# Kernel tuning notes

Hardware: AMD Instinct MI355X
Metric: run time of the kernel (lower is better)

## Reference

```python
import jax, jax.numpy as jnp
import numpy as np

DIM = 1024
HEADS = 16
HEAD_DIM = DIM // HEADS
SCALE = HEAD_DIM ** -0.5
EPS = 1e-5


def layernorm(x, g, b):
    mu = jnp.mean(x, axis=-1, keepdims=True)
    var = jnp.mean((x - mu) ** 2, axis=-1, keepdims=True)
    return (x - mu) * jax.lax.rsqrt(var + EPS) * g + b


def setup_inputs() -> dict:
    key = jax.random.key(0)
    ks = jax.random.split(key, 12)
    B, N = 2, 2048
    s = DIM ** -0.5
    return {
        "q": jax.random.normal(ks[0], (B, N, DIM), jnp.float32),
        "k": jax.random.normal(ks[1], (B, N, DIM), jnp.float32),
        "v": jax.random.normal(ks[2], (B, N, DIM), jnp.float32),
        "gq": jnp.ones((DIM,), jnp.float32), "bq_ln": jnp.zeros((DIM,), jnp.float32),
        "gk": jnp.ones((DIM,), jnp.float32), "bk_ln": jnp.zeros((DIM,), jnp.float32),
        "gv": jnp.ones((DIM,), jnp.float32), "bv_ln": jnp.zeros((DIM,), jnp.float32),
        "Wq": jax.random.normal(ks[3], (DIM, DIM), jnp.float32) * s,
        "bq": jnp.zeros((DIM,), jnp.float32),
        "Wk": jax.random.normal(ks[4], (DIM, DIM), jnp.float32) * s,
        "bk": jnp.zeros((DIM,), jnp.float32),
        "Wv": jax.random.normal(ks[5], (DIM, DIM), jnp.float32) * s,
        "bv": jnp.zeros((DIM,), jnp.float32),
        "Wp": jax.random.normal(ks[6], (DIM, DIM), jnp.float32) * s,
        "bp": jnp.zeros((DIM,), jnp.float32),
    }


def reference(q, k, v, gq, bq_ln, gk, bk_ln, gv, bv_ln, Wq, bq, Wk, bk, Wv, bv, Wp, bp):
    B, Nq, C = q.shape
    Nk, Nv = k.shape[1], v.shape[1]
    qn = layernorm(q, gq, bq_ln)
    kn = layernorm(k, gk, bk_ln)
    vn = layernorm(v, gv, bv_ln)
    # project and split heads -> [B, H, N, hd]
    qh = (qn @ Wq + bq).reshape(B, Nq, HEADS, HEAD_DIM).transpose(0, 2, 1, 3)
    kh = (kn @ Wk + bk).reshape(B, Nk, HEADS, HEAD_DIM).transpose(0, 2, 1, 3)
    vh = (vn @ Wv + bv).reshape(B, Nv, HEADS, HEAD_DIM).transpose(0, 2, 1, 3)
    attn = jnp.einsum("bhqd,bhkd->bhqk", qh, kh) * SCALE
    attn = jax.nn.softmax(attn, axis=-1)
    out = jnp.einsum("bhqk,bhkd->bhqd", attn, vh)
    out = out.transpose(0, 2, 1, 3).reshape(B, Nq, C)
    out = out @ Wp + bp
    return (out, kh, vh)
```

## Files before the change

kernel.cpp:

```cpp
#include <hip/hip_runtime.h>
#include <cstdint>

#define DIMC 1024
#define NSEQ 2048
#define BATCH 2
#define HEADS 16
#define HD 64
#define MROWS (BATCH * NSEQ)

typedef unsigned short u16;
typedef unsigned int u32;
typedef __attribute__((ext_vector_type(8))) short bf16x8;
typedef __attribute__((ext_vector_type(4))) float f32x4;

#if __has_builtin(__builtin_amdgcn_exp2f)
#define EXP2(x) __builtin_amdgcn_exp2f(x)
#else
#define EXP2(x) exp2f(x)
#endif

__device__ __forceinline__ u16 f2bf(float f) {
  union { float f; u32 u; } v; v.f = f;
  u32 u = v.u;
  return (u16)((u + 0x7fffu + ((u >> 16) & 1u)) >> 16);
}
__device__ __forceinline__ u32 pack_rne(float a, float b) {
  return (u32)f2bf(a) | ((u32)f2bf(b) << 16);
}
__device__ __forceinline__ u32 pack_trunc(float a, float b) {
  union { float f; u32 u; } x, y; x.f = a; y.f = b;
  return (x.u >> 16) | (y.u & 0xffff0000u);
}
__device__ __forceinline__ void gload_lds16(const void* g, void* l) {
  __builtin_amdgcn_global_load_lds((const __attribute__((address_space(1))) void*)g,
                                   (__attribute__((address_space(3))) void*)l, 16, 0, 0);
}

__global__ __launch_bounds__(256)
void prep(const float* __restrict__ q, const float* __restrict__ k,
          const float* __restrict__ v,
          const float* __restrict__ gq, const float* __restrict__ bq,
          const float* __restrict__ gk, const float* __restrict__ bk,
          const float* __restrict__ gv, const float* __restrict__ bv,
          const float* __restrict__ w0, const float* __restrict__ w1,
          const float* __restrict__ w2, const float* __restrict__ w3,
          u16* __restrict__ xn, u16* __restrict__ wtout) {
  __shared__ float rs[4], rs2[4];
  __shared__ float tile[32][33];
  int tid = threadIdx.x;
  if (blockIdx.x < 3 * MROWS) {
    int rowid = blockIdx.x;
    int tensor = rowid >> 12;
    int r = rowid & 4095;
    const float *src, *g, *b;
    if (tensor == 0)      { src = q; g = gq; b = bq; }
    else if (tensor == 1) { src = k; g = gk; b = bk; }
    else                  { src = v; g = gv; b = bv; }
    src += (size_t)r * DIMC;
    u16* dst = xn + (size_t)tensor * MROWS * DIMC + (size_t)r * DIMC;
    float4 x = ((const float4*)src)[tid];
    float s  = x.x + x.y + x.z + x.w;
    float s2 = x.x*x.x + x.y*x.y + x.z*x.z + x.w*x.w;
    #pragma unroll
    for (int m = 1; m < 64; m <<= 1) { s += __shfl_xor(s, m); s2 += __shfl_xor(s2, m); }
    int wave = tid >> 6, lane = tid & 63;
    if (lane == 0) { rs[wave] = s; rs2[wave] = s2; }
    __syncthreads();
    s  = rs[0] + rs[1] + rs[2] + rs[3];
    s2 = rs2[0] + rs2[1] + rs2[2] + rs2[3];
    float mu  = s * (1.0f / DIMC);
    float var = s2 * (1.0f / DIMC) - mu * mu;
    float inv = rsqrtf(var + 1e-5f);
    float4 gg = ((const float4*)g)[tid];
    float4 bb = ((const float4*)b)[tid];
    uint2 o;
    o.x = pack_rne((x.x - mu) * inv * gg.x + bb.x, (x.y - mu) * inv * gg.y + bb.y);
    o.y = pack_rne((x.z - mu) * inv * gg.z + bb.z, (x.w - mu) * inv * gg.w + bb.w);
    ((uint2*)dst)[tid] = o;
  } else {
    int blk = blockIdx.x - 3 * MROWS;
    int widx = blk >> 10, t = blk & 1023;
    int ti = t >> 5, tj = t & 31;
    const float* W = (widx == 0) ? w0 : (widx == 1) ? w1 : (widx == 2) ? w2 : w3;
    u16* O = wtout + (size_t)widx * DIMC * DIMC;
    int tx = tid & 31, ty = tid >> 5;
    #pragma unroll
    for (int rr = 0; rr < 32; rr += 8)
      tile[ty + rr][tx] = W[(size_t)(ti * 32 + ty + rr) * DIMC + tj * 32 + tx];
    __syncthreads();
    #pragma unroll
    for (int rr = 0; rr < 32; rr += 8)
      O[(size_t)(tj * 32 + ty + rr) * DIMC + ti * 32 + tx] = f2bf(tile[tx][ty + rr]);
  }
}

__global__ __launch_bounds__(256)
void qkv_gemm(const u16* __restrict__ xn, const u16* __restrict__ wt,
              const float* __restrict__ bq, const float* __restrict__ bk,
              const float* __restrict__ bv,
              float* __restrict__ out, u16* __restrict__ qh,
              u16* __restrict__ khb, u16* __restrict__ vtb) {
  __shared__ u16 smem[128 * 136];
  u16* As = smem;
  u16* Bs = smem + 4096;
  u16* Ls = smem;
  const int z = blockIdx.z;
  const u16* A  = xn + (size_t)z * MROWS * DIMC;
  const u16* Bt = wt + (size_t)z * DIMC * DIMC;
  const float* bias = (z == 0) ? bq : (z == 1) ? bk : bv;
  const int bm = blockIdx.x, bn = blockIdx.y;
  const int tid = threadIdx.x;
  const int wave = tid >> 6, lane = tid & 63;
  const int wm = (wave & 1) * 64, wn = (wave >> 1) * 64;
  const int row = lane & 15, quad = lane >> 4;
  const float QSCL = 0.18033688011112042f;
  f32x4 acc[4][4] = {};
  for (int k0 = 0; k0 < DIMC; k0 += 32) {
    #pragma unroll
    for (int c = 0; c < 2; ++c) {
      int e = c * 2048 + tid * 8;
      int rr = e >> 5, col = e & 31;
      gload_lds16(&A[(size_t)(bm * 128 + rr) * DIMC + k0 + col], &As[e]);
      gload_lds16(&Bt[(size_t)(bn * 128 + rr) * DIMC + k0 + col], &Bs[e]);
    }
    __syncthreads();
    bf16x8 a[4], b[4];
    #pragma unroll
    for (int i = 0; i < 4; ++i)
      a[i] = *(const bf16x8*)(&As[(wm + i * 16 + row) * 32 + quad * 8]);
    #pragma unroll
    for (int j = 0; j < 4; ++j)
      b[j] = *(const bf16x8*)(&Bs[(wn + j * 16 + row) * 32 + quad * 8]);
    #pragma unroll
    for (int i = 0; i < 4; ++i)
      #pragma unroll
      for (int j = 0; j < 4; ++j)
        acc[i][j] = __builtin_amdgcn_mfma_f32_16x16x32_bf16(a[i], b[j], acc[i][j], 0, 0, 0);
    __syncthreads();
  }
  #pragma unroll
  for (int i = 0; i < 4; ++i) {
    #pragma unroll
    for (int j = 0; j < 4; ++j) {
      float val[4];
      #pragma unroll
      for (int r = 0; r < 4; ++r) {
        int m = bm * 128 + wm + i * 16 + quad * 4 + r;
        int c = bn * 128 + wn + j * 16 + row;
        val[r] = acc[i][j][r] + bias[c];
        int b_ = m >> 11, n = m & 2047, h = c >> 6, d = c & 63;
        int bh = b_ * HEADS + h;
        size_t hidx = ((size_t)bh * NSEQ + n) * HD + d;
        if (z == 0) {
          qh[hidx] = f2bf(val[r] * QSCL);
        } else {
          out[(size_t)z * MROWS * DIMC + hidx] = val[r];
          if (z == 1) khb[hidx] = f2bf(val[r]);
        }
      }
      if (z == 2) {
        int ct = wn + j * 16 + row;
        int mt = wm + i * 16 + quad * 4;
        u32* L = (u32*)(&Ls[ct * 136 + mt]);
        L[0] = pack_rne(val[0], val[1]);
        L[1] = pack_rne(val[2], val[3]);
      }
    }
  }
  if (z == 2) {
    __syncthreads();
    int b_ = (bm * 128) >> 11;
    int nbase = (bm * 128) & 2047;
    #pragma unroll
    for (int it = 0; it < 8; ++it) {
      int idx = it * 256 + tid;
      int ct = idx >> 4, ch = idx & 15;
      uint4 y = *(const uint4*)(&Ls[ct * 136 + ch * 8]);
      int c = bn * 128 + ct;
      int h = c >> 6, d = c & 63;
      size_t o = ((size_t)(b_ * HEADS + h) * HD + d) * NSEQ + nbase + ch * 8;
      *(uint4*)(&vtb[o]) = y;
    }
  }
}

__global__ __launch_bounds__(256)
void out_gemm(const u16* __restrict__ A, const u16* __restrict__ Bt,
              const float* __restrict__ bias, float* __restrict__ outf) {
  __shared__ u16 As[64 * 32];
  __shared__ u16 Bs[128 * 32];
  const int bm = blockIdx.x, bn = blockIdx.y;
  const int tid = threadIdx.x;
  const int wave = tid >> 6, lane = tid & 63;
  const int wm = (wave & 1) * 32, wn = (wave >> 1) * 64;
  const int row = lane & 15, quad = lane >> 4;
  f32x4 acc[2][4] = {};
  for (int k0 = 0; k0 < DIMC; k0 += 32) {
    {
      int e = tid * 8;
      int rr = e >> 5, col = e & 31;
      gload_lds16(&A[(size_t)(bm * 64 + rr) * DIMC + k0 + col], &As[e]);
    }
    #pragma unroll
    for (int c = 0; c < 2; ++c) {
      int e = c * 2048 + tid * 8;
      int rr = e >> 5, col = e & 31;
      gload_lds16(&Bt[(size_t)(bn * 128 + rr) * DIMC + k0 + col], &Bs[e]);
    }
    __syncthreads();
    bf16x8 a[2], b[4];
    #pragma unroll
    for (int i = 0; i < 2; ++i)
      a[i] = *(const bf16x8*)(&As[(wm + i * 16 + row) * 32 + quad * 8]);
    #pragma unroll
    for (int j = 0; j < 4; ++j)
      b[j] = *(const bf16x8*)(&Bs[(wn + j * 16 + row) * 32 + quad * 8]);
    #pragma unroll
    for (int i = 0; i < 2; ++i)
      #pragma unroll
      for (int j = 0; j < 4; ++j)
        acc[i][j] = __builtin_amdgcn_mfma_f32_16x16x32_bf16(a[i], b[j], acc[i][j], 0, 0, 0);
    __syncthreads();
  }
  #pragma unroll
  for (int i = 0; i < 2; ++i)
    #pragma unroll
    for (int j = 0; j < 4; ++j)
      #pragma unroll
      for (int r = 0; r < 4; ++r) {
        int m = bm * 64 + wm + i * 16 + quad * 4 + r;
        int c = bn * 128 + wn + j * 16 + row;
        outf[(size_t)m * DIMC + c] = acc[i][j][r] + bias[c];
      }
}

__global__ __launch_bounds__(256)
void attn_fused(const u16* __restrict__ qh, const u16* __restrict__ kh,
                const u16* __restrict__ vt, u16* __restrict__ ao) {
  __shared__ u16 Ks[2][64 * 64];
  __shared__ u16 Vs[2][64 * 64];
  __shared__ u16 Ps[4][2][16 * 40];
  const int flat = blockIdx.x;
  const int bh = (flat & 7) * 4 + ((flat >> 3) & 3);
  const int qtile = flat >> 5;
  const int b = bh >> 4, h = bh & 15;
  const int tid = threadIdx.x;
  const int wave = tid >> 6, lane = tid & 63;
  const int qi = lane & 15, quad = lane >> 4;
  const int sw = qi & 7;
  const size_t base = (size_t)bh * NSEQ * HD;
  bf16x8 qf[2][2];
  #pragma unroll
  for (int qt = 0; qt < 2; ++qt) {
    int qrow = qtile * 128 + wave * 32 + qt * 16 + qi;
    #pragma unroll
    for (int kc2 = 0; kc2 < 2; ++kc2)
      qf[qt][kc2] = *(const bf16x8*)(&qh[base + (size_t)qrow * HD + kc2 * 32 + quad * 8]);
  }
  #pragma unroll
  for (int c = 0; c < 2; ++c) {
    int p = c * 256 + tid;
    int rk = p >> 3, ck = p & 7;
    gload_lds16(&kh[base + (size_t)rk * HD + (ck ^ (rk & 7)) * 8], &Ks[0][p * 8]);
    gload_lds16(&vt[base + (size_t)rk * NSEQ + (ck ^ (rk & 7)) * 8], &Vs[0][p * 8]);
  }
  __syncthreads();
  float li0 = 0.f, li1 = 0.f;
  f32x4 oacc[2][4] = {};
  u16* P0 = &Ps[wave][0][0];
  u16* P1 = &Ps[wave][1][0];
  for (int t = 0; t < NSEQ / 64; ++t) {
    const int cur = t & 1;
    if (t < NSEQ / 64 - 1) {
      #pragma unroll
      for (int c = 0; c < 2; ++c) {
        int p = c * 256 + tid;
        int rk = p >> 3, ck = p & 7;
        gload_lds16(&kh[base + (size_t)((t + 1) * 64 + rk) * HD + (ck ^ (rk & 7)) * 8],
                    &Ks[cur ^ 1][p * 8]);
        gload_lds16(&vt[base + (size_t)rk * NSEQ + (t + 1) * 64 + (ck ^ (rk & 7)) * 8],
                    &Vs[cur ^ 1][p * 8]);
      }
    }
    const u16* Kb = &Ks[cur][0];
    const u16* Vb = &Vs[cur][0];
    #pragma unroll
    for (int kc = 0; kc < 2; ++kc) {
      const u16* kr0 = &Kb[((kc * 2) * 16 + qi) * 64];
      const u16* kr1 = &Kb[((kc * 2 + 1) * 16 + qi) * 64];
      bf16x8 ka0 = *(const bf16x8*)(&kr0[(quad ^ sw) * 8]);
      bf16x8 ka1 = *(const bf16x8*)(&kr0[((4 + quad) ^ sw) * 8]);
      bf16x8 kb0 = *(const bf16x8*)(&kr1[(quad ^ sw) * 8]);
      bf16x8 kb1 = *(const bf16x8*)(&kr1[((4 + quad) ^ sw) * 8]);
      f32x4 s00 = {}, s01 = {}, s10 = {}, s11 = {};
      __builtin_amdgcn_s_setprio(1);
      s00 = __builtin_amdgcn_mfma_f32_16x16x32_bf16(ka0, qf[0][0], s00, 0, 0, 0);
      s00 = __builtin_amdgcn_mfma_f32_16x16x32_bf16(ka1, qf[0][1], s00, 0, 0, 0);
      s01 = __builtin_amdgcn_mfma_f32_16x16x32_bf16(kb0, qf[0][0], s01, 0, 0, 0);
      s01 = __builtin_amdgcn_mfma_f32_16x16x32_bf16(kb1, qf[0][1], s01, 0, 0, 0);
      s10 = __builtin_amdgcn_mfma_f32_16x16x32_bf16(ka0, qf[1][0], s10, 0, 0, 0);
      s10 = __builtin_amdgcn_mfma_f32_16x16x32_bf16(ka1, qf[1][1], s10, 0, 0, 0);
      s11 = __builtin_amdgcn_mfma_f32_16x16x32_bf16(kb0, qf[1][0], s11, 0, 0, 0);
      s11 = __builtin_amdgcn_mfma_f32_16x16x32_bf16(kb1, qf[1][1], s11, 0, 0, 0);
      __builtin_amdgcn_s_setprio(0);
      float a0 = EXP2(s00[0]), a1 = EXP2(s00[1]), a2 = EXP2(s00[2]), a3 = EXP2(s00[3]);
      float a4 = EXP2(s01[0]), a5 = EXP2(s01[1]), a6 = EXP2(s01[2]), a7 = EXP2(s01[3]);
      float b0 = EXP2(s10[0]), b1 = EXP2(s10[1]), b2 = EXP2(s10[2]), b3 = EXP2(s10[3]);
      float b4 = EXP2(s11[0]), b5 = EXP2(s11[1]), b6 = EXP2(s11[2]), b7 = EXP2(s11[3]);
      li0 += ((a0 + a1) + (a2 + a3)) + ((a4 + a5) + (a6 + a7));
      li1 += ((b0 + b1) + (b2 + b3)) + ((b4 + b5) + (b6 + b7));
      {
        uint2 w;
        w.x = pack_trunc(a0, a1); w.y = pack_trunc(a2, a3);
        *(uint2*)(&P0[qi * 40 + quad * 4]) = w;
        w.x = pack_trunc(a4, a5); w.y = pack_trunc(a6, a7);
        *(uint2*)(&P0[qi * 40 + 16 + quad * 4]) = w;
        w.x = pack_trunc(b0, b1); w.y = pack_trunc(b2, b3);
        *(uint2*)(&P1[qi * 40 + quad * 4]) = w;
        w.x = pack_trunc(b4, b5); w.y = pack_trunc(b6, b7);
        *(uint2*)(&P1[qi * 40 + 16 + quad * 4]) = w;
      }
      asm volatile("" ::: "memory");
      bf16x8 pf0 = *(const bf16x8*)(&P0[qi * 40 + quad * 8]);
      bf16x8 pf1 = *(const bf16x8*)(&P1[qi * 40 + quad * 8]);
      __builtin_amdgcn_s_setprio(1);
      #pragma unroll
      for (int dt = 0; dt < 4; ++dt) {
        bf16x8 vf = *(const bf16x8*)(&Vb[(dt * 16 + qi) * 64 + ((kc * 4 + quad) ^ sw) * 8]);
        oacc[0][dt] = __builtin_amdgcn_mfma_f32_16x16x32_bf16(vf, pf0, oacc[0][dt], 0, 0, 0);
        oacc[1][dt] = __builtin_amdgcn_mfma_f32_16x16x32_bf16(vf, pf1, oacc[1][dt], 0, 0, 0);
      }
      __builtin_amdgcn_s_setprio(0);
    }
    __syncthreads();
  }
  li0 += __shfl_xor(li0, 16); li0 += __shfl_xor(li0, 32);
  li1 += __shfl_xor(li1, 16); li1 += __shfl_xor(li1, 32);
  #pragma unroll
  for (int qt = 0; qt < 2; ++qt) {
    float inv = 1.0f / (qt == 0 ? li0 : li1);
    int token = b * NSEQ + qtile * 128 + wave * 32 + qt * 16 + qi;
    #pragma unroll
    for (int dt = 0; dt < 4; ++dt) {
      int col = h * 64 + dt * 16 + quad * 4;
      *(u32*)(&ao[(size_t)token * DIMC + col]) =
          pack_rne(oacc[qt][dt][0] * inv, oacc[qt][dt][1] * inv);
      *(u32*)(&ao[(size_t)token * DIMC + col + 2]) =
          pack_rne(oacc[qt][dt][2] * inv, oacc[qt][dt][3] * inv);
    }
  }
}

extern "C" void kernel_launch(void* const* d_in, const int* in_sizes, int n_in,
                              void* d_out, int out_size, void* d_ws, size_t ws_size,
                              hipStream_t stream) {
  const float* q    = (const float*)d_in[0];
  const float* k    = (const float*)d_in[1];
  const float* v    = (const float*)d_in[2];
  const float* gq   = (const float*)d_in[3];
  const float* bqln = (const float*)d_in[4];
  const float* gk   = (const float*)d_in[5];
  const float* bkln = (const float*)d_in[6];
  const float* gv   = (const float*)d_in[7];
  const float* bvln = (const float*)d_in[8];
  const float* Wq   = (const float*)d_in[9];
  const float* bq   = (const float*)d_in[10];
  const float* Wk   = (const float*)d_in[11];
  const float* bk   = (const float*)d_in[12];
  const float* Wv   = (const float*)d_in[13];
  const float* bv   = (const float*)d_in[14];
  const float* Wp   = (const float*)d_in[15];
  const float* bp   = (const float*)d_in[16];
  float* out = (float*)d_out;

  char* ws = (char*)d_ws;
  u16* xn  = (u16*)(ws);
  u16* wt  = (u16*)(ws + (size_t)25165824);
  u16* qh  = (u16*)(ws + (size_t)33554432);
  u16* khb = (u16*)(ws + (size_t)41943040);
  u16* ao  = (u16*)(ws + (size_t)50331648);
  u16* vtb = (u16*)d_out;

  const size_t WEL = (size_t)DIMC * DIMC;

  prep<<<3 * MROWS + 4096, 256, 0, stream>>>(q, k, v, gq, bqln, gk, bkln, gv, bvln,
                                             Wq, Wk, Wv, Wp, xn, wt);
  qkv_gemm<<<dim3(MROWS / 128, DIMC / 128, 3), 256, 0, stream>>>(
      xn, wt, bq, bk, bv, out, qh, khb, vtb);
  attn_fused<<<dim3((NSEQ / 128) * BATCH * HEADS), 256, 0, stream>>>(qh, khb, vtb, ao);
  out_gemm<<<dim3(MROWS / 64, DIMC / 128), 256, 0, stream>>>(ao, wt + 3 * WEL, bp, out);
}
```

Measured before the change: 244.2 us.

## Load K/V fragments directly from global into registers, dropping LDS staging

The attention kernel no longer stages K and V tiles in shared memory with async global-to-LDS copies and block barriers. Each wave now reads its MFMA K and V fragments straight from global memory into registers, double-buffered one 32-key step ahead. This removes the LDS traffic and the per-tile __syncthreads. In exchange, the four waves of a block each load the same K/V data redundantly, relying on L1/L2 to absorb it, and register pressure rises from holding two sets of fragments.

```diff
diff --git a/kernel.cpp b/kernel.cpp
--- a/kernel.cpp
+++ b/kernel.cpp
@@ -237,8 +237,6 @@
 __global__ __launch_bounds__(256)
 void attn_fused(const u16* __restrict__ qh, const u16* __restrict__ kh,
                 const u16* __restrict__ vt, u16* __restrict__ ao) {
-  __shared__ u16 Ks[2][64 * 64];
-  __shared__ u16 Vs[2][64 * 64];
   __shared__ u16 Ps[4][2][16 * 40];
   const int flat = blockIdx.x;
   const int bh = (flat & 7) * 4 + ((flat >> 3) & 3);
@@ -247,93 +245,93 @@
   const int tid = threadIdx.x;
   const int wave = tid >> 6, lane = tid & 63;
   const int qi = lane & 15, quad = lane >> 4;
-  const int sw = qi & 7;
   const size_t base = (size_t)bh * NSEQ * HD;
   bf16x8 qf[2][2];
   #pragma unroll
   for (int qt = 0; qt < 2; ++qt) {
     int qrow = qtile * 128 + wave * 32 + qt * 16 + qi;
     #pragma unroll
-    for (int kc2 = 0; kc2 < 2; ++kc2)
-      qf[qt][kc2] = *(const bf16x8*)(&qh[base + (size_t)qrow * HD + kc2 * 32 + quad * 8]);
-  }
-  #pragma unroll
-  for (int c = 0; c < 2; ++c) {
-    int p = c * 256 + tid;
-    int rk = p >> 3, ck = p & 7;
-    gload_lds16(&kh[base + (size_t)rk * HD + (ck ^ (rk & 7)) * 8], &Ks[0][p * 8]);
-    gload_lds16(&vt[base + (size_t)rk * NSEQ + (ck ^ (rk & 7)) * 8], &Vs[0][p * 8]);
-  }
-  __syncthreads();
+    for (int dh = 0; dh < 2; ++dh)
+      qf[qt][dh] = *(const bf16x8*)(&qh[base + (size_t)qrow * HD + dh * 32 + quad * 8]);
+  }
+  const u16* kp  = kh + base + qi * HD + quad * 8;
+  const u16* vp0 = vt + base + (size_t)qi * NSEQ + quad * 8;
+  const u16* vp1 = vp0 + 16 * NSEQ;
+  const u16* vp2 = vp0 + 32 * NSEQ;
+  const u16* vp3 = vp0 + 48 * NSEQ;
   float li0 = 0.f, li1 = 0.f;
   f32x4 oacc[2][4] = {};
   u16* P0 = &Ps[wave][0][0];
   u16* P1 = &Ps[wave][1][0];
-  for (int t = 0; t < NSEQ / 64; ++t) {
-    const int cur = t & 1;
-    if (t < NSEQ / 64 - 1) {
-      #pragma unroll
-      for (int c = 0; c < 2; ++c) {
-        int p = c * 256 + tid;
-        int rk = p >> 3, ck = p & 7;
-        gload_lds16(&kh[base + (size_t)((t + 1) * 64 + rk) * HD + (ck ^ (rk & 7)) * 8],
-                    &Ks[cur ^ 1][p * 8]);
-        gload_lds16(&vt[base + (size_t)rk * NSEQ + (t + 1) * 64 + (ck ^ (rk & 7)) * 8],
-                    &Vs[cur ^ 1][p * 8]);
-      }
-    }
-    const u16* Kb = &Ks[cur][0];
-    const u16* Vb = &Vs[cur][0];
-    #pragma unroll
-    for (int kc = 0; kc < 2; ++kc) {
-      const u16* kr0 = &Kb[((kc * 2) * 16 + qi) * 64];
-      const u16* kr1 = &Kb[((kc * 2 + 1) * 16 + qi) * 64];
-      bf16x8 ka0 = *(const bf16x8*)(&kr0[(quad ^ sw) * 8]);
-      bf16x8 ka1 = *(const bf16x8*)(&kr0[((4 + quad) ^ sw) * 8]);
-      bf16x8 kb0 = *(const bf16x8*)(&kr1[(quad ^ sw) * 8]);
-      bf16x8 kb1 = *(const bf16x8*)(&kr1[((4 + quad) ^ sw) * 8]);
-      f32x4 s00 = {}, s01 = {}, s10 = {}, s11 = {};
-      __builtin_amdgcn_s_setprio(1);
-      s00 = __builtin_amdgcn_mfma_f32_16x16x32_bf16(ka0, qf[0][0], s00, 0, 0, 0);
-      s00 = __builtin_amdgcn_mfma_f32_16x16x32_bf16(ka1, qf[0][1], s00, 0, 0, 0);
-      s01 = __builtin_amdgcn_mfma_f32_16x16x32_bf16(kb0, qf[0][0], s01, 0, 0, 0);
-      s01 = __builtin_amdgcn_mfma_f32_16x16x32_bf16(kb1, qf[0][1], s01, 0, 0, 0);
-      s10 = __builtin_amdgcn_mfma_f32_16x16x32_bf16(ka0, qf[1][0], s10, 0, 0, 0);
-      s10 = __builtin_amdgcn_mfma_f32_16x16x32_bf16(ka1, qf[1][1], s10, 0, 0, 0);
-      s11 = __builtin_amdgcn_mfma_f32_16x16x32_bf16(kb0, qf[1][0], s11, 0, 0, 0);
-      s11 = __builtin_amdgcn_mfma_f32_16x16x32_bf16(kb1, qf[1][1], s11, 0, 0, 0);
-      __builtin_amdgcn_s_setprio(0);
-      float a0 = EXP2(s00[0]), a1 = EXP2(s00[1]), a2 = EXP2(s00[2]), a3 = EXP2(s00[3]);
-      float a4 = EXP2(s01[0]), a5 = EXP2(s01[1]), a6 = EXP2(s01[2]), a7 = EXP2(s01[3]);
-      float b0 = EXP2(s10[0]), b1 = EXP2(s10[1]), b2 = EXP2(s10[2]), b3 = EXP2(s10[3]);
-      float b4 = EXP2(s11[0]), b5 = EXP2(s11[1]), b6 = EXP2(s11[2]), b7 = EXP2(s11[3]);
-      li0 += ((a0 + a1) + (a2 + a3)) + ((a4 + a5) + (a6 + a7));
-      li1 += ((b0 + b1) + (b2 + b3)) + ((b4 + b5) + (b6 + b7));
-      {
-        uint2 w;
-        w.x = pack_trunc(a0, a1); w.y = pack_trunc(a2, a3);
-        *(uint2*)(&P0[qi * 40 + quad * 4]) = w;
-        w.x = pack_trunc(a4, a5); w.y = pack_trunc(a6, a7);
-        *(uint2*)(&P0[qi * 40 + 16 + quad * 4]) = w;
-        w.x = pack_trunc(b0, b1); w.y = pack_trunc(b2, b3);
-        *(uint2*)(&P1[qi * 40 + quad * 4]) = w;
-        w.x = pack_trunc(b4, b5); w.y = pack_trunc(b6, b7);
-        *(uint2*)(&P1[qi * 40 + 16 + quad * 4]) = w;
-      }
-      asm volatile("" ::: "memory");
-      bf16x8 pf0 = *(const bf16x8*)(&P0[qi * 40 + quad * 8]);
-      bf16x8 pf1 = *(const bf16x8*)(&P1[qi * 40 + quad * 8]);
-      __builtin_amdgcn_s_setprio(1);
-      #pragma unroll
-      for (int dt = 0; dt < 4; ++dt) {
-        bf16x8 vf = *(const bf16x8*)(&Vb[(dt * 16 + qi) * 64 + ((kc * 4 + quad) ^ sw) * 8]);
-        oacc[0][dt] = __builtin_amdgcn_mfma_f32_16x16x32_bf16(vf, pf0, oacc[0][dt], 0, 0, 0);
-        oacc[1][dt] = __builtin_amdgcn_mfma_f32_16x16x32_bf16(vf, pf1, oacc[1][dt], 0, 0, 0);
-      }
-      __builtin_amdgcn_s_setprio(0);
-    }
-    __syncthreads();
-  }
+  bf16x8 k0A, k1A, k2A, k3A, v0A, v1A, v2A, v3A;
+  bf16x8 k0B, k1B, k2B, k3B, v0B, v1B, v2B, v3B;
+
+#define ALOADF(S) do {                          \
+    k0##S = *(const bf16x8*)(kp);               \
+    k1##S = *(const bf16x8*)(kp + 32);          \
+    k2##S = *(const bf16x8*)(kp + 1024);        \
+    k3##S = *(const bf16x8*)(kp + 1056);        \
+    v0##S = *(const bf16x8*)(vp0);              \
+    v1##S = *(const bf16x8*)(vp1);              \
+    v2##S = *(const bf16x8*)(vp2);              \
+    v3##S = *(const bf16x8*)(vp3);              \
+    kp += 32 * HD; vp0 += 32; vp1 += 32; vp2 += 32; vp3 += 32; \
+  } while (0)
+
+#define AUNIT(S) do {                                                                  \
+    f32x4 s00 = {}, s01 = {}, s10 = {}, s11 = {};                                      \
+    __builtin_amdgcn_s_setprio(1);                                                     \
+    s00 = __builtin_amdgcn_mfma_f32_16x16x32_bf16(k0##S, qf[0][0], s00, 0, 0, 0);      \
+    s00 = __builtin_amdgcn_mfma_f32_16x16x32_bf16(k1##S, qf[0][1], s00, 0, 0, 0);      \
+    s01 = __builtin_amdgcn_mfma_f32_16x16x32_bf16(k2##S, qf[0][0], s01, 0, 0, 0);      \
+    s01 = __builtin_amdgcn_mfma_f32_16x16x32_bf16(k3##S, qf[0][1], s01, 0, 0, 0);      \
+    s10 = __builtin_amdgcn_mfma_f32_16x16x32_bf16(k0##S, qf[1][0], s10, 0, 0, 0);      \
+    s10 = __builtin_amdgcn_mfma_f32_16x16x32_bf16(k1##S, qf[1][1], s10, 0, 0, 0);      \
+    s11 = __builtin_amdgcn_mfma_f32_16x16x32_bf16(k2##S, qf[1][0], s11, 0, 0, 0);      \
+    s11 = __builtin_amdgcn_mfma_f32_16x16x32_bf16(k3##S, qf[1][1], s11, 0, 0, 0);      \
+    __builtin_amdgcn_s_setprio(0);                                                     \
+    float a0 = EXP2(s00[0]), a1 = EXP2(s00[1]), a2 = EXP2(s00[2]), a3 = EXP2(s00[3]);  \
+    float a4 = EXP2(s01[0]), a5 = EXP2(s01[1]), a6 = EXP2(s01[2]), a7 = EXP2(s01[3]);  \
+    float b0 = EXP2(s10[0]), b1 = EXP2(s10[1]), b2 = EXP2(s10[2]), b3 = EXP2(s10[3]);  \
+    float b4 = EXP2(s11[0]), b5 = EXP2(s11[1]), b6 = EXP2(s11[2]), b7 = EXP2(s11[3]);  \
+    li0 += ((a0 + a1) + (a2 + a3)) + ((a4 + a5) + (a6 + a7));                          \
+    li1 += ((b0 + b1) + (b2 + b3)) + ((b4 + b5) + (b6 + b7));                          \
+    {                                                                                  \
+      uint2 w;                                                                         \
+      w.x = pack_trunc(a0, a1); w.y = pack_trunc(a2, a3);                              \
+      *(uint2*)(&P0[qi * 40 + quad * 4]) = w;                                          \
+      w.x = pack_trunc(a4, a5); w.y = pack_trunc(a6, a7);                              \
+      *(uint2*)(&P0[qi * 40 + 16 + quad * 4]) = w;                                     \
+      w.x = pack_trunc(b0, b1); w.y = pack_trunc(b2, b3);                              \
+      *(uint2*)(&P1[qi * 40 + quad * 4]) = w;                                          \
+      w.x = pack_trunc(b4, b5); w.y = pack_trunc(b6, b7);                              \
+      *(uint2*)(&P1[qi * 40 + 16 + quad * 4]) = w;                                     \
+    }                                                                                  \
+    asm volatile("" ::: "memory");       \
+    bf16x8 pf0 = *(const bf16x8*)(&P0[qi * 40 + quad * 8]);                            \
+    bf16x8 pf1 = *(const bf16x8*)(&P1[qi * 40 + quad * 8]);                            \
+    __builtin_amdgcn_s_setprio(1);                                                     \
+    oacc[0][0] = __builtin_amdgcn_mfma_f32_16x16x32_bf16(v0##S, pf0, oacc[0][0], 0, 0, 0); \
+    oacc[1][0] = __builtin_amdgcn_mfma_f32_16x16x32_bf16(v0##S, pf1, oacc[1][0], 0, 0, 0); \
+    oacc[0][1] = __builtin_amdgcn_mfma_f32_16x16x32_bf16(v1##S, pf0, oacc[0][1], 0, 0, 0); \
+    oacc[1][1] = __builtin_amdgcn_mfma_f32_16x16x32_bf16(v1##S, pf1, oacc[1][1], 0, 0, 0); \
+    oacc[0][2] = __builtin_amdgcn_mfma_f32_16x16x32_bf16(v2##S, pf0, oacc[0][2], 0, 0, 0); \
+    oacc[1][2] = __builtin_amdgcn_mfma_f32_16x16x32_bf16(v2##S, pf1, oacc[1][2], 0, 0, 0); \
+    oacc[0][3] = __builtin_amdgcn_mfma_f32_16x16x32_bf16(v3##S, pf0, oacc[0][3], 0, 0, 0); \
+    oacc[1][3] = __builtin_amdgcn_mfma_f32_16x16x32_bf16(v3##S, pf1, oacc[1][3], 0, 0, 0); \
+    __builtin_amdgcn_s_setprio(0);                                                     \
+  } while (0)
+
+  ALOADF(A);
+  for (int u = 0; u < NSEQ / 32; u += 2) {
+    ALOADF(B);
+    AUNIT(A);
+    if (u + 2 < NSEQ / 32) ALOADF(A);
+    AUNIT(B);
+  }
+#undef ALOADF
+#undef AUNIT
+
   li0 += __shfl_xor(li0, 16); li0 += __shfl_xor(li0, 32);
   li1 += __shfl_xor(li1, 16); li1 += __shfl_xor(li1, 32);
   #pragma unroll
```

New measurement: 310.8 us. 27.3% more time.

## Keep softmax probabilities in registers by permuting the V-transpose layout

Applied to the files above, without the earlier changes.

The V-transpose writer in the projection kernel now stores each 8-element chunk as two 4-element halves at permuted key positions. The permutation makes the MFMA output layout of the score tile match the B-operand layout expected by the PV MFMA. The attention kernel can then pack the exp values straight into bf16 register vectors, dropping the per-wave LDS round trip (stores, compiler barrier, reloads) for P. The trade-off is narrower 8-byte scattered global stores in the V writer, and correctness depends on the permutation matching the MFMA lane mapping.

```diff
diff --git a/kernel.cpp b/kernel.cpp
--- a/kernel.cpp
+++ b/kernel.cpp
@@ -178,8 +178,13 @@
       uint4 y = *(const uint4*)(&Ls[ct * 136 + ch * 8]);
       int c = bn * 128 + ct;
       int h = c >> 6, d = c & 63;
-      size_t o = ((size_t)(b_ * HEADS + h) * HD + d) * NSEQ + nbase + ch * 8;
-      *(uint4*)(&vtb[o]) = y;
+      size_t rowb = ((size_t)(b_ * HEADS + h) * HD + d) * NSEQ;
+      int K0 = nbase + ch * 8;
+      int d1 = (K0 & ~31) + ((K0 & 8) ? 16 : 0) + ((K0 & 16) ? 4 : 0);
+      uint2 lo; lo.x = y.x; lo.y = y.y;
+      uint2 hi; hi.x = y.z; hi.y = y.w;
+      *(uint2*)(&vtb[rowb + d1])     = lo;
+      *(uint2*)(&vtb[rowb + d1 + 8]) = hi;
     }
   }
 }
@@ -239,7 +244,6 @@
                 const u16* __restrict__ vt, u16* __restrict__ ao) {
   __shared__ u16 Ks[2][64 * 64];
   __shared__ u16 Vs[2][64 * 64];
-  __shared__ u16 Ps[4][2][16 * 40];
   const int flat = blockIdx.x;
   const int bh = (flat & 7) * 4 + ((flat >> 3) & 3);
   const int qtile = flat >> 5;
@@ -254,8 +258,8 @@
   for (int qt = 0; qt < 2; ++qt) {
     int qrow = qtile * 128 + wave * 32 + qt * 16 + qi;
     #pragma unroll
-    for (int kc2 = 0; kc2 < 2; ++kc2)
-      qf[qt][kc2] = *(const bf16x8*)(&qh[base + (size_t)qrow * HD + kc2 * 32 + quad * 8]);
+    for (int dh = 0; dh < 2; ++dh)
+      qf[qt][dh] = *(const bf16x8*)(&qh[base + (size_t)qrow * HD + dh * 32 + quad * 8]);
   }
   #pragma unroll
   for (int c = 0; c < 2; ++c) {
@@ -267,8 +271,6 @@
   __syncthreads();
   float li0 = 0.f, li1 = 0.f;
   f32x4 oacc[2][4] = {};
-  u16* P0 = &Ps[wave][0][0];
-  u16* P1 = &Ps[wave][1][0];
   for (int t = 0; t < NSEQ / 64; ++t) {
     const int cur = t & 1;
     if (t < NSEQ / 64 - 1) {
@@ -309,26 +311,17 @@
       float b4 = EXP2(s11[0]), b5 = EXP2(s11[1]), b6 = EXP2(s11[2]), b7 = EXP2(s11[3]);
       li0 += ((a0 + a1) + (a2 + a3)) + ((a4 + a5) + (a6 + a7));
       li1 += ((b0 + b1) + (b2 + b3)) + ((b4 + b5) + (b6 + b7));
-      {
-        uint2 w;
-        w.x = pack_trunc(a0, a1); w.y = pack_trunc(a2, a3);
-        *(uint2*)(&P0[qi * 40 + quad * 4]) = w;
-        w.x = pack_trunc(a4, a5); w.y = pack_trunc(a6, a7);
-        *(uint2*)(&P0[qi * 40 + 16 + quad * 4]) = w;
-        w.x = pack_trunc(b0, b1); w.y = pack_trunc(b2, b3);
-        *(uint2*)(&P1[qi * 40 + quad * 4]) = w;
-        w.x = pack_trunc(b4, b5); w.y = pack_trunc(b6, b7);
-        *(uint2*)(&P1[qi * 40 + 16 + quad * 4]) = w;
-      }
-      asm volatile("" ::: "memory");
-      bf16x8 pf0 = *(const bf16x8*)(&P0[qi * 40 + quad * 8]);
-      bf16x8 pf1 = *(const bf16x8*)(&P1[qi * 40 + quad * 8]);
+      union { bf16x8 v; u32 u[4]; } pu0, pu1;
+      pu0.u[0] = pack_trunc(a0, a1); pu0.u[1] = pack_trunc(a2, a3);
+      pu0.u[2] = pack_trunc(a4, a5); pu0.u[3] = pack_trunc(a6, a7);
+      pu1.u[0] = pack_trunc(b0, b1); pu1.u[1] = pack_trunc(b2, b3);
+      pu1.u[2] = pack_trunc(b4, b5); pu1.u[3] = pack_trunc(b6, b7);
       __builtin_amdgcn_s_setprio(1);
       #pragma unroll
       for (int dt = 0; dt < 4; ++dt) {
         bf16x8 vf = *(const bf16x8*)(&Vb[(dt * 16 + qi) * 64 + ((kc * 4 + quad) ^ sw) * 8]);
-        oacc[0][dt] = __builtin_amdgcn_mfma_f32_16x16x32_bf16(vf, pf0, oacc[0][dt], 0, 0, 0);
-        oacc[1][dt] = __builtin_amdgcn_mfma_f32_16x16x32_bf16(vf, pf1, oacc[1][dt], 0, 0, 0);
+        oacc[0][dt] = __builtin_amdgcn_mfma_f32_16x16x32_bf16(vf, pu0.v, oacc[0][dt], 0, 0, 0);
+        oacc[1][dt] = __builtin_amdgcn_mfma_f32_16x16x32_bf16(vf, pu1.v, oacc[1][dt], 0, 0, 0);
       }
       __builtin_amdgcn_s_setprio(0);
     }
```

New measurement: 241.3 us. No clear change (-1.2%).
